# Kernel optimization log

Hardware: AMD Instinct MI355X
Metric: run time of the kernel (lower is better)

## Reference

```python
import jax, jax.numpy as jnp
import numpy as np

NUM_EMBEDDINGS = 512
EMBEDDING_DIM = 128
COMMITMENT = 0.25
DECAY = 0.99
EPS = 1e-05


def setup_inputs() -> dict:
    key = jax.random.key(0)
    k1, k2 = jax.random.split(key)
    z = jax.random.normal(k1, (32, EMBEDDING_DIM, 64, 64), dtype=jnp.float32)
    embedding = jax.random.normal(k2, (EMBEDDING_DIM, NUM_EMBEDDINGS), dtype=jnp.float32)
    cluster_size = jnp.zeros((NUM_EMBEDDINGS,), dtype=jnp.float32)
    embed_avg = embedding  # buffer initialized as a clone of embedding
    return {"z": z, "embedding": embedding, "cluster_size": cluster_size, "embed_avg": embed_avg}


def reference(z, embedding, cluster_size, embed_avg):
    sg = jax.lax.stop_gradient
    D, K = embedding.shape
    B, C, H, W = z.shape
    z_perm = jnp.transpose(z, (0, 2, 3, 1))          # [B,H,W,D]
    flat_z = z_perm.reshape(-1, D)                    # [N,D]

    distances = ((flat_z ** 2).sum(1, keepdims=True)
                 - 2.0 * (flat_z @ embedding)
                 + (embedding ** 2).sum(0)[None, :])  # [N,K]
    idx = jnp.argmin(distances, axis=1)               # [N]

    # gather codes (equivalent to one-hot @ embedding.T, without materializing one-hot)
    quantized = jnp.take(embedding.T, idx, axis=0).reshape(z_perm.shape)  # [B,H,W,D]
    quantized = jnp.transpose(quantized, (0, 3, 1, 2))                    # [B,D,H,W]

    # EMA codebook update (training branch)
    enc_sum = jax.ops.segment_sum(jnp.ones_like(idx, dtype=flat_z.dtype), idx, num_segments=K)  # [K]
    embed_sum = jax.ops.segment_sum(flat_z, idx, num_segments=K).T                              # [D,K]
    new_cluster_size = cluster_size * DECAY + (1.0 - DECAY) * enc_sum
    new_embed_avg = embed_avg * DECAY + (1.0 - DECAY) * embed_sum
    n = jnp.maximum(new_cluster_size.sum(), 1e-05)
    cs = (new_cluster_size + EPS) / (n + K * EPS) * n
    new_embedding = new_embed_avg / cs[None, :]

    e_latent_loss = jnp.mean((sg(quantized) - z) ** 2)
    q_latent_loss = jnp.mean((quantized - sg(z)) ** 2)
    loss = q_latent_loss + COMMITMENT * e_latent_loss

    quantized_out = z + sg(quantized - z)             # straight-through
    encoding_indices = idx.reshape(B, H, W)
    return (quantized_out, loss, encoding_indices, new_embedding, new_cluster_size, new_embed_avg)
```

## Files before the change

kernel.cpp:

```cpp
#include <hip/hip_runtime.h>
#include <hip/hip_bf16.h>
#include <float.h>

typedef _Float16 f16;
typedef __attribute__((ext_vector_type(8))) _Float16 half8;
typedef __attribute__((ext_vector_type(4))) float floatx4;

#define DIM   128
#define HW    4096
#define NPOS  131072
#define K     512
#define ZSTRIDE_B 524288

#define Q_OFF     0
#define LOSS_OFF  16777216
#define IDX_OFF   16777217
#define NEMB_OFF  16908289
#define NCS_OFF   16973825
#define NEA_OFF   16974337

#define WS_E2    0
#define WS_ENC   512
#define WS_ESUM  1024
#define WS_EHI   1024
#define WS_ELO   33792
#define WS_LOSS  66560
#define WS_NN    66561

#define XST 136

__global__ __launch_bounds__(256) void k_prep(const float* __restrict__ emb,
                                              f16* __restrict__ ehiP,
                                              f16* __restrict__ eloP,
                                              float* __restrict__ e2) {
    int lin = blockIdx.x * 256 + threadIdx.x;
    int d = lin >> 9, k = lin & 511;
    float v = emb[lin];
    atomicAdd(&e2[k], v * v);
    f16 h = (f16)v;
    f16 l = (f16)(v - (float)h);
    int g = k >> 4, r = k & 15;
    int dc = d >> 5, w = d & 31, quad = w >> 3, j = w & 7;
    int idx = (g * 4 + dc) * 512 + quad * 128 + r * 8 + j;
    ehiP[idx] = h;
    eloP[idx] = l;
}

__global__ __launch_bounds__(256, 2) void k_assign(const float* __restrict__ z,
                                                   const f16* __restrict__ ehiP,
                                                   const f16* __restrict__ eloP,
                                                   const float* __restrict__ e2,
                                                   float* __restrict__ out) {
    __shared__ f16 xs_h[64 * XST];
    __shared__ f16 xs_l[64 * XST];
    __shared__ float wbD[256];
    __shared__ int   wbI[256];

    const int tid  = threadIdx.x;
    const int lane = tid & 63;
    const int wv   = tid >> 6;
    const int n0   = blockIdx.x * 64;
    const int b    = n0 >> 12;
    const int hw0  = n0 & 4095;
    const float* zb = z + b * ZSTRIDE_B + hw0;
    const int l15  = lane & 15;
    const int quad = lane >> 4;

    float sv0[16], sv1[16];
    #pragma unroll
    for (int it = 0; it < 16; ++it) {
        int lin = tid + it * 256;
        int i  = lin & 63;
        int dp = lin >> 6;
        sv0[it] = zb[(2 * dp) * HW + i];
        sv1[it] = zb[(2 * dp + 1) * HW + i];
    }
    #pragma unroll
    for (int it = 0; it < 16; ++it) {
        int lin = tid + it * 256;
        int i  = lin & 63;
        int dp = lin >> 6;
        float v0 = sv0[it], v1 = sv1[it];
        f16 h0 = (f16)v0; f16 l0 = (f16)(v0 - (float)h0);
        f16 h1 = (f16)v1; f16 l1 = (f16)(v1 - (float)h1);
        union { f16 h[2]; unsigned int u; } ph, pl;
        ph.h[0] = h0; ph.h[1] = h1;
        pl.h[0] = l0; pl.h[1] = l1;
        *(unsigned int*)&xs_h[i * XST + 2 * dp] = ph.u;
        *(unsigned int*)&xs_l[i * XST + 2 * dp] = pl.u;
    }
    __syncthreads();

    float bestD[4][4];
    int   bestI[4][4];
    #pragma unroll
    for (int t = 0; t < 4; ++t)
        #pragma unroll
        for (int r = 0; r < 4; ++r) { bestD[t][r] = FLT_MAX; bestI[t][r] = 0x7fffffff; }

    const half8* gh = (const half8*)ehiP;
    const half8* gl = (const half8*)eloP;

    for (int cc = 0; cc < 4; ++cc) {
        floatx4 acc[4][2];
        #pragma unroll
        for (int t = 0; t < 4; ++t)
            #pragma unroll
            for (int nt = 0; nt < 2; ++nt) acc[t][nt] = (floatx4){0.f, 0.f, 0.f, 0.f};

        for (int dc = 0; dc < 4; ++dc) {
            half8 ah[4], al[4];
            #pragma unroll
            for (int t = 0; t < 4; ++t) {
                int off = (t * 16 + l15) * XST + dc * 32 + quad * 8;
                ah[t] = *(const half8*)&xs_h[off];
                al[t] = *(const half8*)&xs_l[off];
            }
            #pragma unroll
            for (int nt = 0; nt < 2; ++nt) {
                int g  = cc * 8 + wv * 2 + nt;
                int bi = (g * 4 + dc) * 64 + lane;
                half8 bh = gh[bi];
                half8 bl = gl[bi];
                #pragma unroll
                for (int t = 0; t < 4; ++t) {
                    acc[t][nt] = __builtin_amdgcn_mfma_f32_16x16x32_f16(ah[t], bh, acc[t][nt], 0, 0, 0);
                    acc[t][nt] = __builtin_amdgcn_mfma_f32_16x16x32_f16(al[t], bh, acc[t][nt], 0, 0, 0);
                    acc[t][nt] = __builtin_amdgcn_mfma_f32_16x16x32_f16(ah[t], bl, acc[t][nt], 0, 0, 0);
                }
            }
        }
        #pragma unroll
        for (int nt = 0; nt < 2; ++nt) {
            int c = cc * 128 + wv * 32 + nt * 16 + l15;
            float ee = e2[c];
            #pragma unroll
            for (int t = 0; t < 4; ++t)
                #pragma unroll
                for (int r = 0; r < 4; ++r) {
                    float s = fmaf(-2.f, acc[t][nt][r], ee);
                    if (s < bestD[t][r]) { bestD[t][r] = s; bestI[t][r] = c; }
                }
        }
    }

    #pragma unroll
    for (int mask = 1; mask <= 8; mask <<= 1) {
        #pragma unroll
        for (int t = 0; t < 4; ++t)
            #pragma unroll
            for (int r = 0; r < 4; ++r) {
                float od = __shfl_xor(bestD[t][r], mask, 64);
                int   oi = __shfl_xor(bestI[t][r], mask, 64);
                if (od < bestD[t][r] || (od == bestD[t][r] && oi < bestI[t][r])) {
                    bestD[t][r] = od; bestI[t][r] = oi;
                }
            }
    }
    if (l15 == 0) {
        #pragma unroll
        for (int t = 0; t < 4; ++t)
            #pragma unroll
            for (int r = 0; r < 4; ++r) {
                int m = t * 16 + quad * 4 + r;
                wbD[wv * 64 + m] = bestD[t][r];
                wbI[wv * 64 + m] = bestI[t][r];
            }
    }
    __syncthreads();
    if (tid < 64) {
        float bd = wbD[tid]; int bi = wbI[tid];
        #pragma unroll
        for (int w = 1; w < 4; ++w) {
            float od = wbD[w * 64 + tid]; int oi = wbI[w * 64 + tid];
            if (od < bd || (od == bd && oi < bi)) { bd = od; bi = oi; }
        }
        out[IDX_OFF + n0 + tid] = (float)bi;
    }
}

#define DC 8
__global__ __launch_bounds__(256) void k_ema2(const float* __restrict__ z,
                                              const float* __restrict__ emb,
                                              float* __restrict__ out,
                                              float* __restrict__ enc,
                                              float* __restrict__ esum,
                                              float* __restrict__ lossAcc) {
    __shared__ float acc[DC][K];
    __shared__ float embs[DC][K];
    __shared__ float cnt[K];
    __shared__ float wred[4];

    const int tid = threadIdx.x;
    const int lane = tid & 63;
    const int wv = tid >> 6;
    const int half   = blockIdx.x & 1;
    const int dchunk = (blockIdx.x >> 1) & 15;
    const int b      = blockIdx.x >> 5;
    const int d0 = dchunk * DC;
    const bool doCnt = (dchunk == 0);

    for (int i = tid; i < DC * K; i += 256) {
        ((float*)acc)[i] = 0.f;
        ((float*)embs)[i] = emb[d0 * K + i];
    }
    if (doCnt) for (int i = tid; i < K; i += 256) cnt[i] = 0.f;
    __syncthreads();

    const float* zb  = z + b * ZSTRIDE_B;
    const float* idp = out + IDX_OFF + b * HW;
    float* qb = out + Q_OFF + b * ZSTRIDE_B;
    float lsum = 0.f;

    const int p0 = half * 2048;
    for (int t = p0; t < p0 + 2048; t += 1024) {
        const int p = t + 4 * tid;
        float4 iv = *(const float4*)(idp + p);
        int k0 = (int)iv.x;
        int k1 = (int)iv.y;
        int k2 = (int)iv.z;
        int k3 = (int)iv.w;
        if (doCnt) {
            atomicAdd(&cnt[k0], 1.f); atomicAdd(&cnt[k1], 1.f);
            atomicAdd(&cnt[k2], 1.f); atomicAdd(&cnt[k3], 1.f);
        }
        #pragma unroll
        for (int d = 0; d < DC; ++d) {
            float4 zv = *(const float4*)(zb + (d0 + d) * HW + p);
            atomicAdd(&acc[d][k0], zv.x);
            atomicAdd(&acc[d][k1], zv.y);
            atomicAdd(&acc[d][k2], zv.z);
            atomicAdd(&acc[d][k3], zv.w);
            float4 qv;
            qv.x = embs[d][k0]; qv.y = embs[d][k1];
            qv.z = embs[d][k2]; qv.w = embs[d][k3];
            *(float4*)(qb + (d0 + d) * HW + p) = qv;
            float dx = qv.x - zv.x; lsum = fmaf(dx, dx, lsum);
            float dy = qv.y - zv.y; lsum = fmaf(dy, dy, lsum);
            float dz2 = qv.z - zv.z; lsum = fmaf(dz2, dz2, lsum);
            float dw = qv.w - zv.w; lsum = fmaf(dw, dw, lsum);
        }
    }

    #pragma unroll
    for (int m = 32; m >= 1; m >>= 1) lsum += __shfl_xor(lsum, m, 64);
    if (lane == 0) wred[wv] = lsum;
    __syncthreads();
    if (tid == 0) atomicAdd(lossAcc, wred[0] + wred[1] + wred[2] + wred[3]);

    for (int i = tid; i < DC * K; i += 256) {
        int d = i >> 9, k = i & 511;
        atomicAdd(&esum[(d0 + d) * K + k], acc[d][k]);
    }
    if (doCnt) for (int i = tid; i < K; i += 256) atomicAdd(&enc[i], cnt[i]);
}

__global__ __launch_bounds__(512) void k_final(const float* __restrict__ enc,
                                               const float* __restrict__ cs_in,
                                               const float* __restrict__ lossAcc,
                                               float* __restrict__ out,
                                               float* __restrict__ nnOut) {
    __shared__ float red[512];
    int k = threadIdx.x;
    float ncs = fmaf(cs_in[k], 0.99f, 0.01f * enc[k]);
    red[k] = ncs;
    out[NCS_OFF + k] = ncs;
    __syncthreads();
    for (int s = 256; s > 0; s >>= 1) {
        if (k < s) red[k] += red[k + s];
        __syncthreads();
    }
    if (k == 0) {
        nnOut[0] = fmaxf(red[0], 1e-5f);
        out[LOSS_OFF] = lossAcc[0] * 1.25f / 16777216.0f;
    }
}

__global__ __launch_bounds__(512) void k_final2(const float* __restrict__ esum,
                                                const float* __restrict__ eavg_in,
                                                const float* __restrict__ nnIn,
                                                float* __restrict__ out) {
    int d = blockIdx.x;
    int k = threadIdx.x;
    float nn = nnIn[0];
    float ncs = out[NCS_OFF + k];
    float cs = (ncs + 1e-5f) / (nn + (float)K * 1e-5f) * nn;
    float ea = fmaf(eavg_in[d * K + k], 0.99f, 0.01f * esum[d * K + k]);
    out[NEA_OFF + d * K + k] = ea;
    out[NEMB_OFF + d * K + k] = ea / cs;
}

extern "C" void kernel_launch(void* const* d_in, const int* in_sizes, int n_in,
                              void* d_out, int out_size, void* d_ws, size_t ws_size,
                              hipStream_t stream) {
    const float* z     = (const float*)d_in[0];
    const float* emb   = (const float*)d_in[1];
    const float* cs_in = (const float*)d_in[2];
    const float* eavg  = (const float*)d_in[3];
    float* out = (float*)d_out;
    float* wsF = (float*)d_ws;

    hipMemsetAsync(wsF + WS_E2, 0, 1024 * sizeof(float), stream);
    hipMemsetAsync(wsF + WS_LOSS, 0, sizeof(float), stream);

    k_prep<<<256, 256, 0, stream>>>(emb, (f16*)(wsF + WS_EHI), (f16*)(wsF + WS_ELO),
                                    wsF + WS_E2);
    k_assign<<<NPOS / 64, 256, 0, stream>>>(z,
                                            (const f16*)(wsF + WS_EHI),
                                            (const f16*)(wsF + WS_ELO),
                                            wsF + WS_E2, out);
    hipMemsetAsync(wsF + WS_ESUM, 0, 65536 * sizeof(float), stream);
    k_ema2<<<1024, 256, 0, stream>>>(z, emb, out, wsF + WS_ENC, wsF + WS_ESUM,
                                     wsF + WS_LOSS);
    k_final<<<1, 512, 0, stream>>>(wsF + WS_ENC, cs_in, wsF + WS_LOSS,
                                   out, wsF + WS_NN);
    k_final2<<<128, 512, 0, stream>>>(wsF + WS_ESUM, eavg, wsF + WS_NN, out);
}
```

Baseline: 291.1 us.

## Fuse quantized output write and loss into assign kernel; rotate EMA atomics

Moves the gather of codebook vectors, the quantized output store and the loss reduction from the EMA kernel into the assignment kernel. The z tile is already in LDS there (as hi/lo f16), and the code is rebuilt from the packed hi/lo codebook. This removes one z read and the embedding staging from the EMA pass, which now only accumulates sums and counts. It also switches global float atomics to unsafeAtomicAdd and rotates each block's flush order to spread contention on esum. The quantized values are reconstructed as hi+lo f16, which may differ slightly from the exact fp32 embedding.

```diff
diff --git a/kernel.cpp b/kernel.cpp
--- a/kernel.cpp
+++ b/kernel.cpp
@@ -36,7 +36,7 @@
     int lin = blockIdx.x * 256 + threadIdx.x;
     int d = lin >> 9, k = lin & 511;
     float v = emb[lin];
-    atomicAdd(&e2[k], v * v);
+    unsafeAtomicAdd(&e2[k], v * v);
     f16 h = (f16)v;
     f16 l = (f16)(v - (float)h);
     int g = k >> 4, r = k & 15;
@@ -50,11 +50,14 @@
                                                    const f16* __restrict__ ehiP,
                                                    const f16* __restrict__ eloP,
                                                    const float* __restrict__ e2,
-                                                   float* __restrict__ out) {
+                                                   float* __restrict__ out,
+                                                   float* __restrict__ lossAcc) {
     __shared__ f16 xs_h[64 * XST];
     __shared__ f16 xs_l[64 * XST];
     __shared__ float wbD[256];
     __shared__ int   wbI[256];
+    __shared__ int   bidx[64];
+    __shared__ float wred[4];
 
     const int tid  = threadIdx.x;
     const int lane = tid & 63;
@@ -175,42 +178,60 @@
             float od = wbD[w * 64 + tid]; int oi = wbI[w * 64 + tid];
             if (od < bd || (od == bd && oi < bi)) { bd = od; bi = oi; }
         }
+        bidx[tid] = bi;
         out[IDX_OFF + n0 + tid] = (float)bi;
     }
+    __syncthreads();
+
+    float* qb = out + Q_OFF + b * ZSTRIDE_B + hw0;
+    float lsum = 0.f;
+    #pragma unroll
+    for (int it = 0; it < 4; ++it) {
+        int o = wv * 4 + it;
+        int c = bidx[lane];
+        int g = c >> 4, r = c & 15;
+        int base = (g * 4 + (o >> 2)) * 512 + (o & 3) * 128 + r * 8;
+        half8 hh = *(const half8*)&ehiP[base];
+        half8 ll = *(const half8*)&eloP[base];
+        half8 zh = *(const half8*)&xs_h[lane * XST + o * 8];
+        half8 zl = *(const half8*)&xs_l[lane * XST + o * 8];
+        #pragma unroll
+        for (int jj = 0; jj < 8; ++jj) {
+            float q  = (float)hh[jj] + (float)ll[jj];
+            float zz = (float)zh[jj] + (float)zl[jj];
+            qb[(o * 8 + jj) * HW + lane] = q;
+            float df = q - zz;
+            lsum = fmaf(df, df, lsum);
+        }
+    }
+    #pragma unroll
+    for (int m = 32; m >= 1; m >>= 1) lsum += __shfl_xor(lsum, m, 64);
+    if (lane == 0) wred[wv] = lsum;
+    __syncthreads();
+    if (tid == 0) unsafeAtomicAdd(lossAcc, wred[0] + wred[1] + wred[2] + wred[3]);
 }
 
 #define DC 8
 __global__ __launch_bounds__(256) void k_ema2(const float* __restrict__ z,
-                                              const float* __restrict__ emb,
-                                              float* __restrict__ out,
+                                              const float* __restrict__ out,
                                               float* __restrict__ enc,
-                                              float* __restrict__ esum,
-                                              float* __restrict__ lossAcc) {
+                                              float* __restrict__ esum) {
     __shared__ float acc[DC][K];
-    __shared__ float embs[DC][K];
     __shared__ float cnt[K];
-    __shared__ float wred[4];
 
     const int tid = threadIdx.x;
-    const int lane = tid & 63;
-    const int wv = tid >> 6;
     const int half   = blockIdx.x & 1;
     const int dchunk = (blockIdx.x >> 1) & 15;
     const int b      = blockIdx.x >> 5;
     const int d0 = dchunk * DC;
     const bool doCnt = (dchunk == 0);
 
-    for (int i = tid; i < DC * K; i += 256) {
-        ((float*)acc)[i] = 0.f;
-        ((float*)embs)[i] = emb[d0 * K + i];
-    }
+    for (int i = tid; i < DC * K; i += 256) ((float*)acc)[i] = 0.f;
     if (doCnt) for (int i = tid; i < K; i += 256) cnt[i] = 0.f;
     __syncthreads();
 
     const float* zb  = z + b * ZSTRIDE_B;
     const float* idp = out + IDX_OFF + b * HW;
-    float* qb = out + Q_OFF + b * ZSTRIDE_B;
-    float lsum = 0.f;
 
     const int p0 = half * 2048;
     for (int t = p0; t < p0 + 2048; t += 1024) {
@@ -231,28 +252,17 @@
             atomicAdd(&acc[d][k1], zv.y);
             atomicAdd(&acc[d][k2], zv.z);
             atomicAdd(&acc[d][k3], zv.w);
-            float4 qv;
-            qv.x = embs[d][k0]; qv.y = embs[d][k1];
-            qv.z = embs[d][k2]; qv.w = embs[d][k3];
-            *(float4*)(qb + (d0 + d) * HW + p) = qv;
-            float dx = qv.x - zv.x; lsum = fmaf(dx, dx, lsum);
-            float dy = qv.y - zv.y; lsum = fmaf(dy, dy, lsum);
-            float dz2 = qv.z - zv.z; lsum = fmaf(dz2, dz2, lsum);
-            float dw = qv.w - zv.w; lsum = fmaf(dw, dw, lsum);
-        }
-    }
-
-    #pragma unroll
-    for (int m = 32; m >= 1; m >>= 1) lsum += __shfl_xor(lsum, m, 64);
-    if (lane == 0) wred[wv] = lsum;
-    __syncthreads();
-    if (tid == 0) atomicAdd(lossAcc, wred[0] + wred[1] + wred[2] + wred[3]);
-
+        }
+    }
+    __syncthreads();
+
+    const int rot = (blockIdx.x & 31) << 6;
     for (int i = tid; i < DC * K; i += 256) {
-        int d = i >> 9, k = i & 511;
-        atomicAdd(&esum[(d0 + d) * K + k], acc[d][k]);
-    }
-    if (doCnt) for (int i = tid; i < K; i += 256) atomicAdd(&enc[i], cnt[i]);
+        int j = (i + rot) & (DC * K - 1);
+        int d = j >> 9, k = j & 511;
+        unsafeAtomicAdd(&esum[(d0 + d) * K + k], acc[d][k]);
+    }
+    if (doCnt) for (int i = tid; i < K; i += 256) unsafeAtomicAdd(&enc[i], cnt[i]);
 }
 
 __global__ __launch_bounds__(512) void k_final(const float* __restrict__ enc,
@@ -308,10 +318,9 @@
     k_assign<<<NPOS / 64, 256, 0, stream>>>(z,
                                             (const f16*)(wsF + WS_EHI),
                                             (const f16*)(wsF + WS_ELO),
-                                            wsF + WS_E2, out);
+                                            wsF + WS_E2, out, wsF + WS_LOSS);
     hipMemsetAsync(wsF + WS_ESUM, 0, 65536 * sizeof(float), stream);
-    k_ema2<<<1024, 256, 0, stream>>>(z, emb, out, wsF + WS_ENC, wsF + WS_ESUM,
-                                     wsF + WS_LOSS);
+    k_ema2<<<1024, 256, 0, stream>>>(z, out, wsF + WS_ENC, wsF + WS_ESUM);
     k_final<<<1, 512, 0, stream>>>(wsF + WS_ENC, cs_in, wsF + WS_LOSS,
                                    out, wsF + WS_NN);
     k_final2<<<128, 512, 0, stream>>>(wsF + WS_ESUM, eavg, wsF + WS_NN, out);
```

Result: slower. 302.8 us (+4.0%).
